# Kernel tuning notes

Measured on AMD Instinct MI355X. Metric: run time of the kernel, lower is better.

## Reference

```python
import jax, jax.numpy as jnp
import numpy as np

N, M, D = 8192, 8192, 64

def setup_inputs() -> dict:
    key = jax.random.key(0)
    kx, ky = jax.random.split(key)
    x = jax.random.normal(kx, (N, D), dtype=jnp.float32)
    y = jax.random.normal(ky, (M, D), dtype=jnp.float32)
    return {"x": x, "y": y}

def reference(x, y):
    T = 1.0
    # Dmat = 2 - euclidean cdist(x, y), computed via the Gram trick.
    sq = (jnp.sum(x * x, axis=1)[:, None]
          + jnp.sum(y * y, axis=1)[None, :]
          - 2.0 * (x @ y.T))
    Dmat = 2.0 - jnp.sqrt(jnp.maximum(sq, 0.0))          # [N, M]
    logprob_rows = jax.nn.log_softmax(Dmat * T, axis=1)   # [N, M]
    logprob_cols = jax.nn.log_softmax(Dmat.T * T, axis=1) # [M, N]
    choice_rows = jnp.argmax(logprob_rows, axis=1)        # [N]
    choice_cols = jnp.argmax(logprob_cols, axis=1)        # [M]
    seq = jnp.arange(M, dtype=choice_cols.dtype)
    mutual = choice_rows[choice_cols] == seq              # [M] bool
    lp_rows = jnp.take_along_axis(logprob_rows, choice_rows[:, None], axis=1)[:, 0]  # [N]
    lp_cols = jnp.take_along_axis(logprob_cols, choice_cols[:, None], axis=1)[:, 0]  # [M]
    # Padded (jit-friendly) form of the boolean compaction: entries where
    # mutual is False are zeroed; mutual mask identifies valid matches.
    log_probs = jnp.where(mutual, lp_rows[choice_cols] + lp_cols, 0.0)  # [M]
    dmatches = jnp.stack([choice_cols, seq], axis=1)      # [M, 2]
    return (log_probs, dmatches, mutual)
```

## Files before the change

### kernel.cpp

```cpp
#include <hip/hip_runtime.h>
#include <stdint.h>

#define NROWS 8192
#define MCOLS 8192
#define DDIM  64

typedef _Float16 half8   __attribute__((ext_vector_type(8)));
typedef float    floatx4 __attribute__((ext_vector_type(4)));

__device__ __forceinline__ unsigned f2key(float f) {
  unsigned u = __float_as_uint(f);
  return (u & 0x80000000u) ? ~u : (u | 0x80000000u);
}
__device__ __forceinline__ float key2f(unsigned k) {
  unsigned u = (k & 0x80000000u) ? (k & 0x7fffffffu) : ~k;
  return __uint_as_float(u);
}

__global__ void init_kernel(unsigned long long* __restrict__ rk,
                            unsigned long long* __restrict__ ck,
                            float* __restrict__ rs, float* __restrict__ cs) {
  int i = blockIdx.x * 256 + threadIdx.x;
  if (i < NROWS) { rk[i] = 0ull; rs[i] = 0.0f; }
  if (i < MCOLS) { ck[i] = 0ull; cs[i] = 0.0f; }
}

__global__ void norms_kernel(const float* __restrict__ x, const float* __restrict__ y,
                             float* __restrict__ xn, float* __restrict__ yn) {
  int gt   = blockIdx.x * 256 + threadIdx.x;
  int wave = gt >> 6;
  int lane = threadIdx.x & 63;
  const float* src; float* dst; int row;
  if (wave < NROWS) { src = x; dst = xn; row = wave; }
  else              { src = y; dst = yn; row = wave - NROWS; }
  float v = src[(size_t)row * DDIM + lane];
  float s = v * v;
  #pragma unroll
  for (int off = 32; off > 0; off >>= 1) s += __shfl_down(s, off);
  if (lane == 0) dst[row] = s;
}

__global__ void convert_kernel(const float* __restrict__ x, const float* __restrict__ y,
                               _Float16* __restrict__ xh, _Float16* __restrict__ xl,
                               _Float16* __restrict__ yh, _Float16* __restrict__ yl) {
  int gid = blockIdx.x * 256 + threadIdx.x;
  const float* src; _Float16 *dh, *dl; int t;
  if (gid < 65536) { src = x; dh = xh; dl = xl; t = gid; }
  else             { src = y; dh = yh; dl = yl; t = gid - 65536; }
  int lane = t & 63;
  int c    = (t >> 6) & 1;
  int p    = t >> 7;
  int row  = p * 16 + (lane & 15);
  int k0   = c * 32 + ((lane >> 4) << 3);
  const float* s = src + (size_t)row * DDIM + k0;
  _Float16 hbuf[8], lbuf[8];
  #pragma unroll
  for (int j = 0; j < 8; ++j) {
    float f = s[j];
    _Float16 h = (_Float16)f;
    hbuf[j] = h;
    lbuf[j] = (_Float16)((f - (float)h) * 2048.0f);
  }
  size_t o = (size_t)t * 8;
  *(half8*)(dh + o) = *(half8*)hbuf;
  *(half8*)(dl + o) = *(half8*)lbuf;
}

__global__ __launch_bounds__(512, 4) void mfma_tile_kernel(
    const _Float16* __restrict__ xh, const _Float16* __restrict__ xl,
    const _Float16* __restrict__ yh, const _Float16* __restrict__ yl,
    const float* __restrict__ xn, const float* __restrict__ yn,
    unsigned long long* __restrict__ row_key, float* __restrict__ row_sum,
    unsigned long long* __restrict__ col_key, float* __restrict__ col_sum)
{
  __shared__ unsigned long long lkey[256 * 8];
  __shared__ float              lsum[256 * 8];

  const int wave  = threadIdx.x >> 6;
  const int lane  = threadIdx.x & 63;
  const int l15   = lane & 15;
  const int g     = lane >> 4;
  const int ap    = blockIdx.y * 8 + wave;
  const int rbase = ap * 16;

  const size_t abase = (size_t)ap * 128 + lane;
  half8 ah0 = ((const half8*)xh)[abase];
  half8 ah1 = ((const half8*)xh)[abase + 64];
  half8 al0 = ((const half8*)xl)[abase];
  half8 al1 = ((const half8*)xl)[abase + 64];

  float xne[4], rsum[4], rmax[4]; int ridx[4];
  #pragma unroll
  for (int r = 0; r < 4; ++r) {
    xne[r]  = xn[rbase + g * 4 + r];
    rsum[r] = 0.0f; rmax[r] = -3.4e38f; ridx[r] = 0;
  }

  const int cp0 = blockIdx.x * 16;
  const size_t bbase = (size_t)cp0 * 128 + lane;
  half8 nbh0 = ((const half8*)yh)[bbase];
  half8 nbh1 = ((const half8*)yh)[bbase + 64];
  half8 nbl0 = ((const half8*)yl)[bbase];
  half8 nbl1 = ((const half8*)yl)[bbase + 64];

  for (int jt = 0; jt < 16; ++jt) {
    half8 bh0 = nbh0, bh1 = nbh1, bl0 = nbl0, bl1 = nbl1;
    if (jt < 15) {
      size_t nb = bbase + (size_t)(jt + 1) * 128;
      nbh0 = ((const half8*)yh)[nb];  nbh1 = ((const half8*)yh)[nb + 64];
      nbl0 = ((const half8*)yl)[nb];  nbl1 = ((const half8*)yl)[nb + 64];
    }

    floatx4 c1 = {}, c2 = {};
    c1 = __builtin_amdgcn_mfma_f32_16x16x32_f16(ah0, bh0, c1, 0, 0, 0);
    c1 = __builtin_amdgcn_mfma_f32_16x16x32_f16(ah1, bh1, c1, 0, 0, 0);
    c2 = __builtin_amdgcn_mfma_f32_16x16x32_f16(al0, bh0, c2, 0, 0, 0);
    c2 = __builtin_amdgcn_mfma_f32_16x16x32_f16(al1, bh1, c2, 0, 0, 0);
    c2 = __builtin_amdgcn_mfma_f32_16x16x32_f16(ah0, bl0, c2, 0, 0, 0);
    c2 = __builtin_amdgcn_mfma_f32_16x16x32_f16(ah1, bl1, c2, 0, 0, 0);

    const int col = cp0 * 16 + jt * 16 + l15;
    const float ync = yn[col];
    float csum = 0.0f, cmax = -3.4e38f; int cidx = 0;

    #pragma unroll
    for (int r = 0; r < 4; ++r) {
      float dot = fmaf(c2[r], (1.0f / 2048.0f), c1[r]);
      float sq  = fmaxf(fmaf(-2.0f, dot, xne[r] + ync), 0.0f);
      float d   = 2.0f - sqrtf(sq);
      float e   = __expf(d);
      rsum[r] += e;  csum += e;
      if (d > rmax[r]) { rmax[r] = d; ridx[r] = col; }
      if (d > cmax)    { cmax = d;    cidx = rbase + g * 4 + r; }
    }

    unsigned long long ck =
        ((unsigned long long)f2key(cmax) << 32) | (unsigned long long)(unsigned)(~(unsigned)cidx);
    #pragma unroll
    for (int off = 16; off < 64; off <<= 1) {
      csum += __shfl_xor(csum, off);
      unsigned long long o = __shfl_xor(ck, off);
      if (o > ck) ck = o;
    }
    if (g == 0) {
      int lc = jt * 16 + l15;
      lkey[lc * 8 + wave] = ck;
      lsum[lc * 8 + wave] = csum;
    }
  }

  unsigned long long rk[4];
  #pragma unroll
  for (int r = 0; r < 4; ++r)
    rk[r] = ((unsigned long long)f2key(rmax[r]) << 32) |
            (unsigned long long)(unsigned)(~(unsigned)ridx[r]);
  #pragma unroll
  for (int off = 1; off < 16; off <<= 1) {
    #pragma unroll
    for (int r = 0; r < 4; ++r) {
      rsum[r] += __shfl_xor(rsum[r], off);
      unsigned long long o = __shfl_xor(rk[r], off);
      if (o > rk[r]) rk[r] = o;
    }
  }
  if (l15 == 0) {
    #pragma unroll
    for (int r = 0; r < 4; ++r) {
      atomicMax(row_key + rbase + g * 4 + r, rk[r]);
      atomicAdd(row_sum + rbase + g * 4 + r, rsum[r]);
    }
  }

  __syncthreads();
  int t = threadIdx.x;
  if (t < 256) {
    unsigned long long k = lkey[t * 8];
    float s = lsum[t * 8];
    #pragma unroll
    for (int w = 1; w < 8; ++w) {
      unsigned long long o = lkey[t * 8 + w];
      if (o > k) k = o;
      s += lsum[t * 8 + w];
    }
    int col = blockIdx.x * 256 + t;
    atomicMax(col_key + col, k);
    atomicAdd(col_sum + col, s);
  }
}

__global__ void finalize_kernel(const unsigned long long* __restrict__ row_key,
                                const float* __restrict__ row_sum,
                                const unsigned long long* __restrict__ col_key,
                                const float* __restrict__ col_sum,
                                float* __restrict__ out)
{
  int j = blockIdx.x * 256 + threadIdx.x;
  if (j >= MCOLS) return;
  unsigned long long ck = col_key[j];
  int   ci   = (int)(~(unsigned)ck);
  float cmax = key2f((unsigned)(ck >> 32));
  float lp_col = cmax - logf(col_sum[j]);

  unsigned long long rk = row_key[ci];
  int   rj   = (int)(~(unsigned)rk);
  float rmax = key2f((unsigned)(rk >> 32));
  float lp_row = rmax - logf(row_sum[ci]);

  int mut = (rj == j);
  out[j]                 = mut ? (lp_row + lp_col) : 0.0f;
  out[MCOLS + 2 * j + 0] = (float)ci;
  out[MCOLS + 2 * j + 1] = (float)j;
  out[3 * MCOLS + j]     = mut ? 1.0f : 0.0f;
}

extern "C" void kernel_launch(void* const* d_in, const int* in_sizes, int n_in,
                              void* d_out, int out_size, void* d_ws, size_t ws_size,
                              hipStream_t stream) {
  const float* x = (const float*)d_in[0];
  const float* y = (const float*)d_in[1];
  float* out = (float*)d_out;

  char* ws = (char*)d_ws;
  unsigned long long* row_key = (unsigned long long*)(ws);
  unsigned long long* col_key = (unsigned long long*)(ws + 65536);
  float* row_sum = (float*)(ws + 131072);
  float* col_sum = (float*)(ws + 163840);
  float* xn      = (float*)(ws + 196608);
  float* yn      = (float*)(ws + 229376);
  _Float16* xh = (_Float16*)(ws + 262144);
  _Float16* xl = (_Float16*)(ws + 262144 + 1048576);
  _Float16* yh = (_Float16*)(ws + 262144 + 2097152);
  _Float16* yl = (_Float16*)(ws + 262144 + 3145728);

  convert_kernel<<<512, 256, 0, stream>>>(x, y, xh, xl, yh, yl);
  norms_kernel<<<4096, 256, 0, stream>>>(x, y, xn, yn);
  init_kernel<<<32, 256, 0, stream>>>(row_key, col_key, row_sum, col_sum);
  dim3 grid(MCOLS / 256, NROWS / 128);
  mfma_tile_kernel<<<grid, 512, 0, stream>>>(xh, xl, yh, yl, xn, yn,
                                             row_key, row_sum, col_key, col_sum);
  finalize_kernel<<<32, 256, 0, stream>>>(row_key, row_sum, col_key, col_sum, out);
}
```

Before: 148.2 us.

## Fuse prep kernels and give each wave two row panels per B tile

```diff
diff --git a/kernel.cpp b/kernel.cpp
--- a/kernel.cpp
+++ b/kernel.cpp
@@ -17,174 +17,166 @@
   return __uint_as_float(u);
 }
 
-__global__ void init_kernel(unsigned long long* __restrict__ rk,
-                            unsigned long long* __restrict__ ck,
-                            float* __restrict__ rs, float* __restrict__ cs) {
-  int i = blockIdx.x * 256 + threadIdx.x;
-  if (i < NROWS) { rk[i] = 0ull; rs[i] = 0.0f; }
-  if (i < MCOLS) { ck[i] = 0ull; cs[i] = 0.0f; }
-}
-
-__global__ void norms_kernel(const float* __restrict__ x, const float* __restrict__ y,
-                             float* __restrict__ xn, float* __restrict__ yn) {
-  int gt   = blockIdx.x * 256 + threadIdx.x;
-  int wave = gt >> 6;
-  int lane = threadIdx.x & 63;
-  const float* src; float* dst; int row;
-  if (wave < NROWS) { src = x; dst = xn; row = wave; }
-  else              { src = y; dst = yn; row = wave - NROWS; }
-  float v = src[(size_t)row * DDIM + lane];
-  float s = v * v;
-  #pragma unroll
-  for (int off = 32; off > 0; off >>= 1) s += __shfl_down(s, off);
-  if (lane == 0) dst[row] = s;
-}
-
 __global__ void convert_kernel(const float* __restrict__ x, const float* __restrict__ y,
                                _Float16* __restrict__ xh, _Float16* __restrict__ xl,
-                               _Float16* __restrict__ yh, _Float16* __restrict__ yl) {
-  int gid = blockIdx.x * 256 + threadIdx.x;
-  const float* src; _Float16 *dh, *dl; int t;
-  if (gid < 65536) { src = x; dh = xh; dl = xl; t = gid; }
-  else             { src = y; dh = yh; dl = yl; t = gid - 65536; }
-  int lane = t & 63;
-  int c    = (t >> 6) & 1;
-  int p    = t >> 7;
-  int row  = p * 16 + (lane & 15);
-  int k0   = c * 32 + ((lane >> 4) << 3);
+                               _Float16* __restrict__ yh, _Float16* __restrict__ yl,
+                               float* __restrict__ xn, float* __restrict__ yn,
+                               unsigned long long* __restrict__ rk,
+                               unsigned long long* __restrict__ ck,
+                               float* __restrict__ rs, float* __restrict__ cs) {
+  __shared__ float lnorm[32];
+  const int gid = blockIdx.x * 256 + threadIdx.x;
+  if (gid < 8192) { rk[gid] = 0ull; rs[gid] = 0.0f; ck[gid] = 0ull; cs[gid] = 0.0f; }
+  if (threadIdx.x < 32) lnorm[threadIdx.x] = 0.0f;
+  __syncthreads();
+
+  const float* src; _Float16 *dh, *dl; float* nout; int t, rowbase;
+  if (gid < 65536) { src = x; dh = xh; dl = xl; nout = xn; t = gid;
+                     rowbase = blockIdx.x * 32; }
+  else             { src = y; dh = yh; dl = yl; nout = yn; t = gid - 65536;
+                     rowbase = (blockIdx.x - 256) * 32; }
+
+  const int lane = t & 63;
+  const int c    = (t >> 6) & 1;
+  const int p    = t >> 7;
+  const int row  = p * 16 + (lane & 15);
+  const int k0   = c * 32 + ((lane >> 4) << 3);
   const float* s = src + (size_t)row * DDIM + k0;
+
   _Float16 hbuf[8], lbuf[8];
+  float s8 = 0.0f;
   #pragma unroll
   for (int j = 0; j < 8; ++j) {
     float f = s[j];
     _Float16 h = (_Float16)f;
     hbuf[j] = h;
     lbuf[j] = (_Float16)((f - (float)h) * 2048.0f);
+    s8 = fmaf(f, f, s8);
   }
   size_t o = (size_t)t * 8;
   *(half8*)(dh + o) = *(half8*)hbuf;
   *(half8*)(dl + o) = *(half8*)lbuf;
-}
-
-__global__ __launch_bounds__(512, 4) void mfma_tile_kernel(
+
+  atomicAdd(&lnorm[((p & 1) << 4) | (t & 15)], s8);
+  __syncthreads();
+  if (threadIdx.x < 32) nout[rowbase + threadIdx.x] = lnorm[threadIdx.x];
+}
+
+__global__ __launch_bounds__(256, 4) void mfma_tile_kernel(
     const _Float16* __restrict__ xh, const _Float16* __restrict__ xl,
     const _Float16* __restrict__ yh, const _Float16* __restrict__ yl,
     const float* __restrict__ xn, const float* __restrict__ yn,
     unsigned long long* __restrict__ row_key, float* __restrict__ row_sum,
     unsigned long long* __restrict__ col_key, float* __restrict__ col_sum)
 {
-  __shared__ unsigned long long lkey[256 * 8];
-  __shared__ float              lsum[256 * 8];
-
-  const int wave  = threadIdx.x >> 6;
-  const int lane  = threadIdx.x & 63;
-  const int l15   = lane & 15;
-  const int g     = lane >> 4;
-  const int ap    = blockIdx.y * 8 + wave;
-  const int rbase = ap * 16;
-
-  const size_t abase = (size_t)ap * 128 + lane;
-  half8 ah0 = ((const half8*)xh)[abase];
-  half8 ah1 = ((const half8*)xh)[abase + 64];
-  half8 al0 = ((const half8*)xl)[abase];
-  half8 al1 = ((const half8*)xl)[abase + 64];
-
-  float xne[4], rsum[4], rmax[4]; int ridx[4];
-  #pragma unroll
-  for (int r = 0; r < 4; ++r) {
-    xne[r]  = xn[rbase + g * 4 + r];
-    rsum[r] = 0.0f; rmax[r] = -3.4e38f; ridx[r] = 0;
-  }
-
-  const int cp0 = blockIdx.x * 16;
-  const size_t bbase = (size_t)cp0 * 128 + lane;
-  half8 nbh0 = ((const half8*)yh)[bbase];
-  half8 nbh1 = ((const half8*)yh)[bbase + 64];
-  half8 nbl0 = ((const half8*)yl)[bbase];
-  half8 nbl1 = ((const half8*)yl)[bbase + 64];
+  __shared__ unsigned long long lkey[256];
+  __shared__ float              lsum[256];
+
+  const int wave = threadIdx.x >> 6;
+  const int lane = threadIdx.x & 63;
+  const int l15  = lane & 15;
+  const int g    = lane >> 4;
+  const int ap0  = blockIdx.y * 8 + wave * 2;
+  const int ro   = ap0 * 16 + g * 4;
+  const int colbase = blockIdx.x * 256;
+
+  lkey[threadIdx.x] = 0ull;
+  lsum[threadIdx.x] = 0.0f;
+  __syncthreads();
+
+  const half8* xh8 = (const half8*)xh;
+  const half8* xl8 = (const half8*)xl;
+  const half8* yh8 = (const half8*)yh;
+  const half8* yl8 = (const half8*)yl;
+  const size_t a0 = (size_t)ap0 * 128 + lane;
+  half8 Ah[2][2], Al[2][2];
+  #pragma unroll
+  for (int p = 0; p < 2; ++p) {
+    Ah[p][0] = xh8[a0 + p * 128];      Ah[p][1] = xh8[a0 + p * 128 + 64];
+    Al[p][0] = xl8[a0 + p * 128];      Al[p][1] = xl8[a0 + p * 128 + 64];
+  }
+
+  float xne[8], rsum[8], rmax[8]; int ridx[8];
+  #pragma unroll
+  for (int s = 0; s < 8; ++s) {
+    xne[s]  = xn[ro + ((s >> 2) << 4) + (s & 3)];
+    rsum[s] = 0.0f; rmax[s] = -3.4e38f; ridx[s] = 0;
+  }
 
   for (int jt = 0; jt < 16; ++jt) {
-    half8 bh0 = nbh0, bh1 = nbh1, bl0 = nbl0, bl1 = nbl1;
-    if (jt < 15) {
-      size_t nb = bbase + (size_t)(jt + 1) * 128;
-      nbh0 = ((const half8*)yh)[nb];  nbh1 = ((const half8*)yh)[nb + 64];
-      nbl0 = ((const half8*)yl)[nb];  nbl1 = ((const half8*)yl)[nb + 64];
+    const size_t b0 = (size_t)(blockIdx.x * 16 + jt) * 128 + lane;
+    const half8 bh0 = yh8[b0], bh1 = yh8[b0 + 64];
+    const half8 bl0 = yl8[b0], bl1 = yl8[b0 + 64];
+    const int col = colbase + jt * 16 + l15;
+    const float ync = yn[col];
+
+    float dv[8], ev[8];
+    #pragma unroll
+    for (int p = 0; p < 2; ++p) {
+      floatx4 c1 = {}, c2 = {};
+      c1 = __builtin_amdgcn_mfma_f32_16x16x32_f16(Ah[p][0], bh0, c1, 0, 0, 0);
+      c1 = __builtin_amdgcn_mfma_f32_16x16x32_f16(Ah[p][1], bh1, c1, 0, 0, 0);
+      c2 = __builtin_amdgcn_mfma_f32_16x16x32_f16(Al[p][0], bh0, c2, 0, 0, 0);
+      c2 = __builtin_amdgcn_mfma_f32_16x16x32_f16(Al[p][1], bh1, c2, 0, 0, 0);
+      c2 = __builtin_amdgcn_mfma_f32_16x16x32_f16(Ah[p][0], bl0, c2, 0, 0, 0);
+      c2 = __builtin_amdgcn_mfma_f32_16x16x32_f16(Ah[p][1], bl1, c2, 0, 0, 0);
+      #pragma unroll
+      for (int r = 0; r < 4; ++r) {
+        const int s = p * 4 + r;
+        float dot = fmaf(c2[r], (1.0f / 2048.0f), c1[r]);
+        float sq  = fmaxf(fmaf(-2.0f, dot, xne[s] + ync), 0.0f);
+        float d   = 2.0f - __builtin_amdgcn_sqrtf(sq);
+        float e   = __expf(d);
+        rsum[s] += e;
+        if (d > rmax[s]) ridx[s] = col;
+        rmax[s] = fmaxf(rmax[s], d);
+        dv[s] = d; ev[s] = e;
+      }
     }
 
-    floatx4 c1 = {}, c2 = {};
-    c1 = __builtin_amdgcn_mfma_f32_16x16x32_f16(ah0, bh0, c1, 0, 0, 0);
-    c1 = __builtin_amdgcn_mfma_f32_16x16x32_f16(ah1, bh1, c1, 0, 0, 0);
-    c2 = __builtin_amdgcn_mfma_f32_16x16x32_f16(al0, bh0, c2, 0, 0, 0);
-    c2 = __builtin_amdgcn_mfma_f32_16x16x32_f16(al1, bh1, c2, 0, 0, 0);
-    c2 = __builtin_amdgcn_mfma_f32_16x16x32_f16(ah0, bl0, c2, 0, 0, 0);
-    c2 = __builtin_amdgcn_mfma_f32_16x16x32_f16(ah1, bl1, c2, 0, 0, 0);
-
-    const int col = cp0 * 16 + jt * 16 + l15;
-    const float ync = yn[col];
-    float csum = 0.0f, cmax = -3.4e38f; int cidx = 0;
-
-    #pragma unroll
-    for (int r = 0; r < 4; ++r) {
-      float dot = fmaf(c2[r], (1.0f / 2048.0f), c1[r]);
-      float sq  = fmaxf(fmaf(-2.0f, dot, xne[r] + ync), 0.0f);
-      float d   = 2.0f - sqrtf(sq);
-      float e   = __expf(d);
-      rsum[r] += e;  csum += e;
-      if (d > rmax[r]) { rmax[r] = d; ridx[r] = col; }
-      if (d > cmax)    { cmax = d;    cidx = rbase + g * 4 + r; }
-    }
-
-    unsigned long long ck =
-        ((unsigned long long)f2key(cmax) << 32) | (unsigned long long)(unsigned)(~(unsigned)cidx);
-    #pragma unroll
-    for (int off = 16; off < 64; off <<= 1) {
-      csum += __shfl_xor(csum, off);
-      unsigned long long o = __shfl_xor(ck, off);
-      if (o > ck) ck = o;
-    }
-    if (g == 0) {
-      int lc = jt * 16 + l15;
-      lkey[lc * 8 + wave] = ck;
-      lsum[lc * 8 + wave] = csum;
-    }
-  }
-
-  unsigned long long rk[4];
-  #pragma unroll
-  for (int r = 0; r < 4; ++r)
-    rk[r] = ((unsigned long long)f2key(rmax[r]) << 32) |
-            (unsigned long long)(unsigned)(~(unsigned)ridx[r]);
+    float m01 = fmaxf(dv[0], dv[1]); int i01 = dv[1] > dv[0] ? 1 : 0;
+    float m23 = fmaxf(dv[2], dv[3]); int i23 = dv[3] > dv[2] ? 3 : 2;
+    float m45 = fmaxf(dv[4], dv[5]); int i45 = dv[5] > dv[4] ? 5 : 4;
+    float m67 = fmaxf(dv[6], dv[7]); int i67 = dv[7] > dv[6] ? 7 : 6;
+    float mA  = fmaxf(m01, m23);     int iA  = m23 > m01 ? i23 : i01;
+    float mB  = fmaxf(m45, m67);     int iB  = m67 > m45 ? i67 : i45;
+    float mC  = fmaxf(mA, mB);       int iC  = mB  > mA  ? iB  : iA;
+    int crow  = ro + ((iC >> 2) << 4) + (iC & 3);
+    float csum = ((ev[0] + ev[1]) + (ev[2] + ev[3])) + ((ev[4] + ev[5]) + (ev[6] + ev[7]));
+    unsigned long long ckey =
+        ((unsigned long long)f2key(mC) << 32) | (unsigned long long)(unsigned)(~(unsigned)crow);
+    atomicMax(&lkey[jt * 16 + l15], ckey);
+    atomicAdd(&lsum[jt * 16 + l15], csum);
+  }
+
+  unsigned long long rkk[8];
+  #pragma unroll
+  for (int s = 0; s < 8; ++s)
+    rkk[s] = ((unsigned long long)f2key(rmax[s]) << 32) |
+             (unsigned long long)(unsigned)(~(unsigned)ridx[s]);
   #pragma unroll
   for (int off = 1; off < 16; off <<= 1) {
     #pragma unroll
-    for (int r = 0; r < 4; ++r) {
-      rsum[r] += __shfl_xor(rsum[r], off);
-      unsigned long long o = __shfl_xor(rk[r], off);
-      if (o > rk[r]) rk[r] = o;
+    for (int s = 0; s < 8; ++s) {
+      rsum[s] += __shfl_xor(rsum[s], off);
+      unsigned long long o = __shfl_xor(rkk[s], off);
+      if (o > rkk[s]) rkk[s] = o;
     }
   }
   if (l15 == 0) {
     #pragma unroll
-    for (int r = 0; r < 4; ++r) {
-      atomicMax(row_key + rbase + g * 4 + r, rk[r]);
-      atomicAdd(row_sum + rbase + g * 4 + r, rsum[r]);
+    for (int s = 0; s < 8; ++s) {
+      int row = ro + ((s >> 2) << 4) + (s & 3);
+      atomicMax(row_key + row, rkk[s]);
+      atomicAdd(row_sum + row, rsum[s]);
     }
   }
 
   __syncthreads();
-  int t = threadIdx.x;
-  if (t < 256) {
-    unsigned long long k = lkey[t * 8];
-    float s = lsum[t * 8];
-    #pragma unroll
-    for (int w = 1; w < 8; ++w) {
-      unsigned long long o = lkey[t * 8 + w];
-      if (o > k) k = o;
-      s += lsum[t * 8 + w];
-    }
-    int col = blockIdx.x * 256 + t;
-    atomicMax(col_key + col, k);
-    atomicAdd(col_sum + col, s);
+  {
+    int col = colbase + threadIdx.x;
+    atomicMax(col_key + col, lkey[threadIdx.x]);
+    atomicAdd(col_sum + col, lsum[threadIdx.x]);
   }
 }
 
@@ -232,11 +224,10 @@
   _Float16* yh = (_Float16*)(ws + 262144 + 2097152);
   _Float16* yl = (_Float16*)(ws + 262144 + 3145728);
 
-  convert_kernel<<<512, 256, 0, stream>>>(x, y, xh, xl, yh, yl);
-  norms_kernel<<<4096, 256, 0, stream>>>(x, y, xn, yn);
-  init_kernel<<<32, 256, 0, stream>>>(row_key, col_key, row_sum, col_sum);
+  convert_kernel<<<512, 256, 0, stream>>>(x, y, xh, xl, yh, yl, xn, yn,
+                                          row_key, col_key, row_sum, col_sum);
   dim3 grid(MCOLS / 256, NROWS / 128);
-  mfma_tile_kernel<<<grid, 512, 0, stream>>>(xh, xl, yh, yl, xn, yn,
+  mfma_tile_kernel<<<grid, 256, 0, stream>>>(xh, xl, yh, yl, xn, yn,
                                              row_key, row_sum, col_key, col_sum);
   finalize_kernel<<<32, 256, 0, stream>>>(row_key, row_sum, col_key, col_sum, out);
 }
```

Measured after the change: 128.3 us. -13.4%, faster.
